# Kernel optimization log

Hardware: AMD Instinct MI355X
Metric: run time of the kernel (lower is better)

Reference implementation:

```python
import jax, jax.numpy as jnp
import numpy as np

ITEM_NUM = 50000
TARGET_ITEM_NUM = 50000
EMB = 128
N_LAYERS = 3
N_EDGES = 800000
N_NODES = ITEM_NUM + 1  # forward uses item_emb[:item_num+1]


def gcn_conv(x, row, col, W, b, n):
    """PyG GCNConv: symmetric-normalized aggregation with self-loops.
    out = D^{-1/2} (A + I) D^{-1/2} (x @ W) + b
    """
    h = x @ W  # [n, d]
    loops = jnp.arange(n)
    r = jnp.concatenate([row, loops])  # source
    c = jnp.concatenate([col, loops])  # target
    deg = jax.ops.segment_sum(jnp.ones(r.shape[0], x.dtype), c, num_segments=n)
    dinv = jnp.where(deg > 0, deg ** -0.5, jnp.zeros_like(deg))
    norm = dinv[r] * dinv[c]  # [E+n]
    out = jax.ops.segment_sum(h[r] * norm[:, None], c, num_segments=n)
    return out + b


def setup_inputs() -> dict:
    key = jax.random.key(0)
    k0, k1, k2 = jax.random.split(key, 3)
    edge_index = jax.random.randint(k0, (2, N_EDGES), 0, N_NODES)
    total = ITEM_NUM + TARGET_ITEM_NUM + 1
    # xavier_uniform for embedding table and per-layer GCN weights
    lim_e = float(np.sqrt(6.0 / (total + EMB)))
    item_emb = jax.random.uniform(k1, (total, EMB), jnp.float32, -lim_e, lim_e)
    lim_w = float(np.sqrt(6.0 / (EMB + EMB)))
    W = jax.random.uniform(k2, (N_LAYERS, EMB, EMB), jnp.float32, -lim_w, lim_w)
    b = jnp.zeros((N_LAYERS, EMB), jnp.float32)
    return {"edge_index": edge_index, "item_emb": item_emb, "W": W, "b": b}


def reference(edge_index, item_emb, W, b):
    n = N_NODES
    row, col = edge_index[0], edge_index[1]
    embeds = [item_emb[:n]]
    for i in range(N_LAYERS):
        embeds.append(gcn_conv(embeds[-1], row, col, W[i], b[i], n))
    return sum(embeds)  # [n, EMB], sum over layer embeddings
```

## Files before the change

### kernel.cpp

```cpp
#include <hip/hip_runtime.h>
#include <hip/hip_bf16.h>


constexpr int NN   = 50001;
constexpr int D    = 128;
constexpr int NPAD = 50048;
constexpr int NBK  = 196;
constexpr int CAP  = 5120;

using bf16x8 = __attribute__((ext_vector_type(8))) short;
using f32x4  = __attribute__((ext_vector_type(4))) float;
using f32x2  = __attribute__((ext_vector_type(2))) float;

__device__ __forceinline__ ushort f2b(float f) {
    unsigned u = __float_as_uint(f);
    return (ushort)((u + 0x7FFFu + ((u >> 16) & 1u)) >> 16);
}
__device__ __forceinline__ float b2f(ushort u) {
    return __uint_as_float((unsigned)u << 16);
}

__global__ __launch_bounds__(256)
void k_build(const int* __restrict__ row, const int* __restrict__ col,
             int* __restrict__ partCur, unsigned* __restrict__ part,
             const float* __restrict__ W, ushort* __restrict__ Wt,
             const float* __restrict__ emb, ushort* __restrict__ xb, int E, int n) {
    int b = blockIdx.x, t = threadIdx.x;
    if (b < NBK) {
        __shared__ int hist[256];
        __shared__ int base[256];
        hist[t] = 0;
        __syncthreads();
        int e0 = b * 4096;
        unsigned rec[16];
        int bkt[16];
#pragma unroll
        for (int k = 0; k < 16; k++) {
            int e = e0 + k * 256 + t;
            if (e < E) {
                int r = row[e], c = col[e];
                rec[k] = (unsigned)r | ((unsigned)(c & 255) << 16);
                bkt[k] = c >> 8;
                atomicAdd(&hist[bkt[k]], 1);
            } else bkt[k] = -1;
        }
        __syncthreads();
        if (hist[t] > 0) base[t] = t * CAP + atomicAdd(&partCur[t], hist[t]);
        __syncthreads();
#pragma unroll
        for (int k = 0; k < 16; k++) {
            if (bkt[k] >= 0) {
                int pos = atomicAdd(&base[bkt[k]], 1);
                if (pos < (bkt[k] + 1) * CAP) part[pos] = rec[k];
            }
        }
    } else if (b < NBK + 192) {
        int idx = (b - NBK) * 256 + t;
        int l = idx >> 14, rem = idx & 16383;
        int c = rem >> 7, k = rem & 127;
        Wt[idx] = f2b(W[l * D * D + k * D + c]);
    } else {
        int i4 = (b - NBK - 192) * 256 + t;
        if (i4 >= NPAD * (D / 4)) return;
        int r = i4 >> 5;
        if (r < n) {
            float4 v = ((const float4*)emb)[i4];
            ushort4 o; o.x = f2b(v.x); o.y = f2b(v.y); o.z = f2b(v.z); o.w = f2b(v.w);
            ((ushort4*)xb)[i4] = o;
        } else {
            ((ushort4*)xb)[i4] = make_ushort4(0, 0, 0, 0);
        }
    }
}

__global__ __launch_bounds__(256)
void k_scat(const unsigned* __restrict__ part, const int* __restrict__ partCur,
            float* __restrict__ dinv, unsigned* __restrict__ rp,
            ushort* __restrict__ meta, int n) {
    __shared__ int hist[256];
    __shared__ int sm[256];
    __shared__ int off[256];
    __shared__ int cur[256];
    int b = blockIdx.x, t = threadIdx.x;
    int node0 = b * 256;
    int nn = min(256, n - node0);
    int T = min(partCur[b], CAP);
    const unsigned* pb = part + (size_t)b * CAP;
    hist[t] = 0;
    __syncthreads();
    for (int i = t; i < T; i += 256) atomicAdd(&hist[pb[i] >> 16], 1);
    __syncthreads();
    int v = hist[t];
    sm[t] = v;
    __syncthreads();
    for (int ofs = 1; ofs < 256; ofs <<= 1) {
        int u = (t >= ofs) ? sm[t - ofs] : 0;
        __syncthreads();
        sm[t] += u;
        __syncthreads();
    }
    off[t] = sm[t] - v;
    cur[t] = 0;
    if (t < nn) {
        dinv[node0 + t] = rsqrtf((float)v + 1.0f);
        rp[node0 + t] = (unsigned)(b * CAP + off[t]) | ((unsigned)v << 20);
    }
    __syncthreads();
    for (int i = t; i < T; i += 256) {
        unsigned rec = pb[i];
        int dl = (int)(rec >> 16);
        int pos = off[dl] + atomicAdd(&cur[dl], 1);
        meta[(size_t)b * CAP + pos] = (ushort)(rec & 0xFFFFu);
    }
}

constexpr int WT_LD = 136;
__global__ __launch_bounds__(256)
void k_gemm_mfma(const ushort* __restrict__ xb, const ushort* __restrict__ WtL,
                 const float* __restrict__ dinv, ushort* __restrict__ h, int n) {
    __shared__ ushort wlds[D * WT_LD];
    for (int idx = threadIdx.x; idx < D * (D / 8); idx += 256) {
        int r = idx >> 4, c8 = (idx & 15) * 8;
        *(uint4*)&wlds[r * WT_LD + c8] = *(const uint4*)&WtL[r * D + c8];
    }
    __syncthreads();

    int wave = threadIdx.x >> 6, lane = threadIdx.x & 63;
    int q = lane >> 4, i = lane & 15;
    int waveRow = blockIdx.x * 128 + wave * 32;

    bf16x8 a[2][4];
#pragma unroll
    for (int rt = 0; rt < 2; rt++) {
        const ushort* base = &xb[(size_t)(waveRow + rt * 16 + i) * D + q * 8];
#pragma unroll
        for (int ks = 0; ks < 4; ks++)
            a[rt][ks] = *(const bf16x8*)(base + ks * 32);
    }

    f32x4 acc[2][8] = {};
#pragma unroll
    for (int ct = 0; ct < 8; ct++) {
        const ushort* wbase = &wlds[(ct * 16 + i) * WT_LD + q * 8];
#pragma unroll
        for (int ks = 0; ks < 4; ks++) {
            bf16x8 bfr = *(const bf16x8*)(wbase + ks * 32);
            acc[0][ct] = __builtin_amdgcn_mfma_f32_16x16x32_bf16(a[0][ks], bfr, acc[0][ct], 0, 0, 0);
            acc[1][ct] = __builtin_amdgcn_mfma_f32_16x16x32_bf16(a[1][ks], bfr, acc[1][ct], 0, 0, 0);
        }
    }

#pragma unroll
    for (int rt = 0; rt < 2; rt++)
#pragma unroll
        for (int r4 = 0; r4 < 4; r4++) {
            int row = waveRow + rt * 16 + q * 4 + r4;
            if (row < n) {
                float dv = dinv[row];
#pragma unroll
                for (int ct = 0; ct < 8; ct++)
                    h[(size_t)row * D + ct * 16 + i] = f2b(acc[rt][ct][r4] * dv);
            }
        }
}

__global__ __launch_bounds__(256)
void k_pull(const unsigned* __restrict__ rp, const ushort* __restrict__ meta,
            const ushort* __restrict__ h,
            const float* __restrict__ dinv, const float* __restrict__ bias,
            ushort* __restrict__ xb_out,
            const float* __restrict__ emb, const ushort* __restrict__ x1,
            const ushort* __restrict__ x2, float* __restrict__ out,
            int n, int mode) {
    int node = (int)((blockIdx.x * 256 + threadIdx.x) >> 6);
    int lane = threadIdx.x & 63;
    if (node >= n) return;
    unsigned pk = rp[node];
    int s = (int)(pk & 0xFFFFFu);
    int e = s + (int)(pk >> 20);
    float ax = 0.f, ay = 0.f;
    int j = s;
    for (; j + 8 <= e; j += 8) {
        ushort  m[8];
        ushort2 v[8];
#pragma unroll
        for (int u = 0; u < 8; u++) m[u] = meta[j + u];
#pragma unroll
        for (int u = 0; u < 8; u++)
            v[u] = *(const ushort2*)&h[(size_t)m[u] * D + 2 * lane];
#pragma unroll
        for (int u = 0; u < 8; u++) {
            ax += b2f(v[u].x);
            ay += b2f(v[u].y);
        }
    }
    for (; j < e; j++) {
        ushort2 v = *(const ushort2*)&h[(size_t)meta[j] * D + 2 * lane];
        ax += b2f(v.x);
        ay += b2f(v.y);
    }
    float di = dinv[node];
    ushort2 sv = *(const ushort2*)&h[(size_t)node * D + 2 * lane];
    float2  bb = ((const float2*)bias)[lane];
    ax = fmaf(ax + b2f(sv.x), di, bb.x);
    ay = fmaf(ay + b2f(sv.y), di, bb.y);
    size_t o = (size_t)node * 64 + lane;
    if (mode == 0) {
        ushort2 xv; xv.x = f2b(ax); xv.y = f2b(ay);
        ((ushort2*)xb_out)[o] = xv;
    } else {
        float2  ev = ((const float2*)emb)[o];
        ushort2 v1 = ((const ushort2*)x1)[o];
        ushort2 v2 = ((const ushort2*)x2)[o];
        f32x2 r;
        r[0] = ev.x + b2f(v1.x) + b2f(v2.x) + ax;
        r[1] = ev.y + b2f(v1.y) + b2f(v2.y) + ay;
        __builtin_nontemporal_store(r, (f32x2*)out + o);
    }
}

extern "C" void kernel_launch(void* const* d_in, const int* in_sizes, int n_in,
                              void* d_out, int out_size, void* d_ws, size_t ws_size,
                              hipStream_t stream) {
    const int*   edge = (const int*)d_in[0];
    const float* emb  = (const float*)d_in[1];
    const float* W    = (const float*)d_in[2];
    const float* b    = (const float*)d_in[3];
    float* out = (float*)d_out;

    const int E = in_sizes[0] / 2;
    const int n = NN;
    const int* row = edge;
    const int* col = edge + E;

    char* ws = (char*)d_ws;
    size_t off = 0;
    auto carve = [&](size_t bytes) { char* p = ws + off; off = (off + bytes + 511) / 512 * 512; return p; };
    int*      partCur = (int*)     carve(256 * 4);
    unsigned* part    = (unsigned*)carve((size_t)NBK * CAP * 4);
    ushort*   meta    = (ushort*)  carve((size_t)NBK * CAP * 2);
    unsigned* rp      = (unsigned*)carve((size_t)n * 4);
    float*    dinv    = (float*)   carve((size_t)n * 4);
    ushort*   Wt      = (ushort*)  carve((size_t)3 * D * D * 2);
    ushort*   xb0     = (ushort*)  carve((size_t)NPAD * D * 2);
    ushort*   xb1     = (ushort*)  carve((size_t)NPAD * D * 2);
    ushort*   xb2     = (ushort*)  carve((size_t)NPAD * D * 2);
    ushort*   h       = (ushort*)  carve((size_t)NPAD * D * 2);

    (void)hipMemsetAsync(partCur, 0, 256 * 4, stream);

    const int init_blocks  = (NPAD * (D / 4) + 255) / 256;
    const int build_blocks = NBK + 192 + init_blocks;
    k_build<<<build_blocks, 256, 0, stream>>>(row, col, partCur, part, W, Wt, emb, xb0, E, n);
    k_scat <<<NBK, 256, 0, stream>>>(part, partCur, dinv, rp, meta, n);

    const int gemm_blocks = NPAD / 128;
    const int pull_blocks = (n + 3) / 4;
    ushort* xin[3]  = {xb0, xb1, xb2};
    ushort* xout[3] = {xb1, xb2, nullptr};
    for (int l = 0; l < 3; l++) {
        k_gemm_mfma<<<gemm_blocks, 256, 0, stream>>>(xin[l], Wt + (size_t)l * D * D, dinv, h, n);
        k_pull<<<pull_blocks, 256, 0, stream>>>(rp, meta, h,
                                                dinv, b + (size_t)l * D, xout[l],
                                                emb, xb1, xb2, out, n, (l < 2) ? 0 : 1);
    }
}
```

Baseline: 279.4 us.

## Pad CSR neighbor lists to multiples of 8 and gather with 16 lanes per node

Neighbor segments in each bucket are padded to multiples of eight and filled with a zero-row index, which removes the remainder loop and allows 128-bit meta loads. The pull kernel now gives each node 16 lanes that each load 16 bytes per neighbor, instead of 64 lanes loading 4 bytes each. The GEMM writes zeros into the padding rows, and the pull kernel zeroes the padded xb rows. The bucket capacity grows to hold the padding, and the wider row-pointer packing leaves fewer bits for the degree.

```diff
diff --git a/kernel.cpp b/kernel.cpp
--- a/kernel.cpp
+++ b/kernel.cpp
@@ -6,11 +6,14 @@
 constexpr int D    = 128;
 constexpr int NPAD = 50048;
 constexpr int NBK  = 196;
-constexpr int CAP  = 5120;
+constexpr int CAP  = 6400;
+constexpr int ZROW = NPAD - 1;
 
 using bf16x8 = __attribute__((ext_vector_type(8))) short;
 using f32x4  = __attribute__((ext_vector_type(4))) float;
 using f32x2  = __attribute__((ext_vector_type(2))) float;
+using u16x8  = __attribute__((ext_vector_type(8))) unsigned short;
+using u32x4  = __attribute__((ext_vector_type(4))) unsigned;
 
 __device__ __forceinline__ ushort f2b(float f) {
     unsigned u = __float_as_uint(f);
@@ -91,7 +94,8 @@
     for (int i = t; i < T; i += 256) atomicAdd(&hist[pb[i] >> 16], 1);
     __syncthreads();
     int v = hist[t];
-    sm[t] = v;
+    int pv = (v + 7) & ~7;
+    sm[t] = pv;
     __syncthreads();
     for (int ofs = 1; ofs < 256; ofs <<= 1) {
         int u = (t >= ofs) ? sm[t - ofs] : 0;
@@ -99,11 +103,11 @@
         sm[t] += u;
         __syncthreads();
     }
-    off[t] = sm[t] - v;
+    off[t] = sm[t] - pv;
     cur[t] = 0;
     if (t < nn) {
         dinv[node0 + t] = rsqrtf((float)v + 1.0f);
-        rp[node0 + t] = (unsigned)(b * CAP + off[t]) | ((unsigned)v << 20);
+        rp[node0 + t] = (unsigned)(b * CAP + off[t]) | ((unsigned)v << 21);
     }
     __syncthreads();
     for (int i = t; i < T; i += 256) {
@@ -112,6 +116,8 @@
         int pos = off[dl] + atomicAdd(&cur[dl], 1);
         meta[(size_t)b * CAP + pos] = (ushort)(rec & 0xFFFFu);
     }
+    for (int p = v; p < pv; p++)
+        meta[(size_t)b * CAP + off[t] + p] = (ushort)ZROW;
 }
 
 constexpr int WT_LD = 136;
@@ -155,12 +161,10 @@
 #pragma unroll
         for (int r4 = 0; r4 < 4; r4++) {
             int row = waveRow + rt * 16 + q * 4 + r4;
-            if (row < n) {
-                float dv = dinv[row];
-#pragma unroll
-                for (int ct = 0; ct < 8; ct++)
-                    h[(size_t)row * D + ct * 16 + i] = f2b(acc[rt][ct][r4] * dv);
-            }
+            float dv = (row < n) ? dinv[row] : 0.f;
+#pragma unroll
+            for (int ct = 0; ct < 8; ct++)
+                h[(size_t)row * D + ct * 16 + i] = f2b(acc[rt][ct][r4] * dv);
         }
 }
 
@@ -172,50 +176,74 @@
             const float* __restrict__ emb, const ushort* __restrict__ x1,
             const ushort* __restrict__ x2, float* __restrict__ out,
             int n, int mode) {
-    int node = (int)((blockIdx.x * 256 + threadIdx.x) >> 6);
-    int lane = threadIdx.x & 63;
-    if (node >= n) return;
+    int node = blockIdx.x * 16 + (threadIdx.x >> 4);
+    int l    = threadIdx.x & 15;
+    if (node >= n) {
+        if (mode == 0) {
+            u16x8 z = {0, 0, 0, 0, 0, 0, 0, 0};
+            *(u16x8*)(xb_out + (size_t)node * D + (l << 3)) = z;
+        }
+        return;
+    }
     unsigned pk = rp[node];
-    int s = (int)(pk & 0xFFFFFu);
-    int e = s + (int)(pk >> 20);
-    float ax = 0.f, ay = 0.f;
-    int j = s;
-    for (; j + 8 <= e; j += 8) {
-        ushort  m[8];
-        ushort2 v[8];
-#pragma unroll
-        for (int u = 0; u < 8; u++) m[u] = meta[j + u];
-#pragma unroll
-        for (int u = 0; u < 8; u++)
-            v[u] = *(const ushort2*)&h[(size_t)m[u] * D + 2 * lane];
+    int s   = (int)(pk & 0x1FFFFFu);
+    int deg = (int)(pk >> 21);
+
+    const ushort* hl = h + (l << 3);
+    float acc[8];
+    {
+        u32x4 v = *(const u32x4*)(hl + (size_t)node * D);
+#pragma unroll
+        for (int k = 0; k < 4; k++) {
+            acc[2 * k]     = __uint_as_float(v[k] << 16);
+            acc[2 * k + 1] = __uint_as_float(v[k] & 0xFFFF0000u);
+        }
+    }
+    for (int j = 0; j < deg; j += 8) {
+        u16x8 mm = *(const u16x8*)&meta[s + j];
 #pragma unroll
         for (int u = 0; u < 8; u++) {
-            ax += b2f(v[u].x);
-            ay += b2f(v[u].y);
-        }
-    }
-    for (; j < e; j++) {
-        ushort2 v = *(const ushort2*)&h[(size_t)meta[j] * D + 2 * lane];
-        ax += b2f(v.x);
-        ay += b2f(v.y);
+            u32x4 v = *(const u32x4*)(hl + (size_t)mm[u] * D);
+#pragma unroll
+            for (int k = 0; k < 4; k++) {
+                acc[2 * k]     += __uint_as_float(v[k] << 16);
+                acc[2 * k + 1] += __uint_as_float(v[k] & 0xFFFF0000u);
+            }
+        }
     }
     float di = dinv[node];
-    ushort2 sv = *(const ushort2*)&h[(size_t)node * D + 2 * lane];
-    float2  bb = ((const float2*)bias)[lane];
-    ax = fmaf(ax + b2f(sv.x), di, bb.x);
-    ay = fmaf(ay + b2f(sv.y), di, bb.y);
-    size_t o = (size_t)node * 64 + lane;
+    const float4* bp = (const float4*)(bias + (l << 3));
+    float4 b0 = bp[0], b1 = bp[1];
+    float r0 = fmaf(acc[0], di, b0.x);
+    float r1 = fmaf(acc[1], di, b0.y);
+    float r2 = fmaf(acc[2], di, b0.z);
+    float r3 = fmaf(acc[3], di, b0.w);
+    float r4 = fmaf(acc[4], di, b1.x);
+    float r5 = fmaf(acc[5], di, b1.y);
+    float r6 = fmaf(acc[6], di, b1.z);
+    float r7 = fmaf(acc[7], di, b1.w);
+    size_t o = (size_t)node * D + (l << 3);
     if (mode == 0) {
-        ushort2 xv; xv.x = f2b(ax); xv.y = f2b(ay);
-        ((ushort2*)xb_out)[o] = xv;
+        u16x8 w;
+        w[0] = f2b(r0); w[1] = f2b(r1); w[2] = f2b(r2); w[3] = f2b(r3);
+        w[4] = f2b(r4); w[5] = f2b(r5); w[6] = f2b(r6); w[7] = f2b(r7);
+        *(u16x8*)(xb_out + o) = w;
     } else {
-        float2  ev = ((const float2*)emb)[o];
-        ushort2 v1 = ((const ushort2*)x1)[o];
-        ushort2 v2 = ((const ushort2*)x2)[o];
-        f32x2 r;
-        r[0] = ev.x + b2f(v1.x) + b2f(v2.x) + ax;
-        r[1] = ev.y + b2f(v1.y) + b2f(v2.y) + ay;
-        __builtin_nontemporal_store(r, (f32x2*)out + o);
+        const float4* ep = (const float4*)(emb + o);
+        float4 e0 = ep[0], e1 = ep[1];
+        u16x8 w1 = *(const u16x8*)(x1 + o);
+        u16x8 w2 = *(const u16x8*)(x2 + o);
+        f32x4 o0, o1;
+        o0[0] = e0.x + b2f(w1[0]) + b2f(w2[0]) + r0;
+        o0[1] = e0.y + b2f(w1[1]) + b2f(w2[1]) + r1;
+        o0[2] = e0.z + b2f(w1[2]) + b2f(w2[2]) + r2;
+        o0[3] = e0.w + b2f(w1[3]) + b2f(w2[3]) + r3;
+        o1[0] = e1.x + b2f(w1[4]) + b2f(w2[4]) + r4;
+        o1[1] = e1.y + b2f(w1[5]) + b2f(w2[5]) + r5;
+        o1[2] = e1.z + b2f(w1[6]) + b2f(w2[6]) + r6;
+        o1[3] = e1.w + b2f(w1[7]) + b2f(w2[7]) + r7;
+        __builtin_nontemporal_store(o0, (f32x4*)(out + o));
+        __builtin_nontemporal_store(o1, (f32x4*)(out + o) + 1);
     }
 }
 
@@ -255,7 +283,7 @@
     k_scat <<<NBK, 256, 0, stream>>>(part, partCur, dinv, rp, meta, n);
 
     const int gemm_blocks = NPAD / 128;
-    const int pull_blocks = (n + 3) / 4;
+    const int pull_blocks = NPAD / 16;
     ushort* xin[3]  = {xb0, xb1, xb2};
     ushort* xout[3] = {xb1, xb2, nullptr};
     for (int l = 0; l < 3; l++) {
```

Result: faster. 245.3 us (-12.2%).
